# Kernel optimization log

Measured on AMD Instinct MI355X. Metric: run time of the kernel, lower is better.

## Reference

```python
import jax, jax.numpy as jnp
import numpy as np

NUM_LEVELS = 4
RADIUS = 4


def _bilinear_zeros(img, x, y):
    """Bilinear sample img (N,H,W) at absolute pixel coords x,y (N,S,S),
    zeros padding outside, matching torch grid_sample(align_corners=True,
    padding_mode='zeros') with absolute->normalized->absolute roundtrip."""
    N, H, W = img.shape
    x0 = jnp.floor(x); y0 = jnp.floor(y)
    x1 = x0 + 1.0;     y1 = y0 + 1.0
    wx1 = x - x0; wx0 = 1.0 - wx1
    wy1 = y - y0; wy0 = 1.0 - wy1
    flat = img.reshape(N, H * W)

    def gather(xi, yi):
        valid = (xi >= 0) & (xi <= W - 1) & (yi >= 0) & (yi <= H - 1)
        xc = jnp.clip(xi, 0, W - 1).astype(jnp.int32)
        yc = jnp.clip(yi, 0, H - 1).astype(jnp.int32)
        idx = (yc * W + xc).reshape(N, -1)
        v = jnp.take_along_axis(flat, idx, axis=1).reshape(xi.shape)
        return jnp.where(valid, v, jnp.zeros((), img.dtype))

    return (wy0 * wx0 * gather(x0, y0) + wy0 * wx1 * gather(x1, y0)
            + wy1 * wx0 * gather(x0, y1) + wy1 * wx1 * gather(x1, y1))


def _avg_pool2(v):
    N, H, W = v.shape
    return v.reshape(N, H // 2, 2, W // 2, 2).mean(axis=(2, 4))


def setup_inputs() -> dict:
    key = jax.random.key(0)
    k1, k2, k3 = jax.random.split(key, 3)
    B, M, C, H, W = 2, 4096, 256, 64, 64
    fmap1 = jax.random.normal(k1, (B, M, C), dtype=jnp.float32)
    fmap2 = jax.random.normal(k2, (B, C, H, W), dtype=jnp.float32)
    u = jax.random.uniform(k3, (B, M, 2), dtype=jnp.float32)
    centroids_coords = u * jnp.array([W - 1, H - 1], dtype=jnp.float32)
    return {"fmap1": fmap1, "fmap2": fmap2, "centroids_coords": centroids_coords}


def reference(fmap1, fmap2, centroids_coords):
    B, M, C = fmap1.shape
    _, _, H, W = fmap2.shape
    side = 2 * RADIUS + 1

    # correlation volume: (B, M, H, W) -> (B*M, H, W)
    corr = jnp.einsum('bmc,bchw->bmhw', fmap1, fmap2).reshape(B * M, H, W)

    d = jnp.arange(-RADIUS, RADIUS + 1, dtype=centroids_coords.dtype)
    di, dj = jnp.meshgrid(d, d, indexing='ij')
    delta = jnp.stack([di, dj], axis=-1)  # (S, S, 2): ch0 = x-offset, ch1 = y-offset

    c = centroids_coords.reshape(B * M, 1, 1, 2)
    vol = corr
    feats = []
    for lvl in range(NUM_LEVELS):
        sc = c + delta                        # (B*M, S, S, 2)
        sampled = _bilinear_zeros(vol, sc[..., 0], sc[..., 1])
        feats.append(sampled.reshape(B, M, side * side))
        c = c / 2.0
        if lvl < NUM_LEVELS - 1:
            vol = _avg_pool2(vol)
    # (B, M, num_levels*S*S) -> (B, out_channels, M)
    return jnp.concatenate(feats, axis=-1).transpose(0, 2, 1)
```

## Files before the change

kernel.cpp:

```cpp
#include <hip/hip_runtime.h>
#include <stdint.h>
#include <stddef.h>

static constexpr int Bb = 2;
static constexpr int Mq = 4096;
static constexpr int Cc = 256;
static constexpr int Hh = 64, Ww = 64;
static constexpr int Np = Hh * Ww;
static constexpr int NL1 = 1024;
static constexpr int RAD = 4;
static constexpr int SIDE = 2 * RAD + 1;
static constexpr int KPL = SIDE * SIDE;
static constexpr int NLVL = 4;
static constexpr int KTOT = NLVL * KPL;

static constexpr size_t WINBUF_B = 0;
static constexpr size_t ABF_B    = WINBUF_B + (size_t)Bb * Mq * 400 * 4;
static constexpr size_t BT_B     = ABF_B + (size_t)Bb * Mq * Cc * 2;
static constexpr size_t B1T_B    = BT_B + (size_t)Bb * Np * Cc * 2;
static constexpr size_t B2T_B    = B1T_B + (size_t)Bb * NL1 * Cc * 2;
static constexpr size_t B3T_B    = B2T_B + (size_t)Bb * 256 * Cc * 2;

typedef float floatx4 __attribute__((ext_vector_type(4)));
typedef short shortx8 __attribute__((ext_vector_type(8)));

union BfPack {
    shortx8 v;
    unsigned short u[8];
};

__device__ __forceinline__ unsigned short f2bf(float f) {
    unsigned int x = __float_as_uint(f);
    x += 0x7fffu + ((x >> 16) & 1u);
    return (unsigned short)(x >> 16);
}

__device__ __forceinline__ float bf2f(unsigned short u) {
    return __uint_as_float((unsigned int)u << 16);
}

__global__ __launch_bounds__(256)
void cvt_kernel(const float* __restrict__ f1, const float* __restrict__ f2,
                unsigned short* __restrict__ Abf, unsigned short* __restrict__ Bt,
                unsigned short* __restrict__ B1t)
{
    __shared__ float tile[64 * 132];
    const int tid = threadIdx.x;
    if (blockIdx.x < 1024) {
        const int t = blockIdx.x * 256 + tid;
        const float4 v0 = *(const float4*)(f1 + (size_t)t * 8);
        const float4 v1 = *(const float4*)(f1 + (size_t)t * 8 + 4);
        BfPack p;
        p.u[0] = f2bf(v0.x); p.u[1] = f2bf(v0.y);
        p.u[2] = f2bf(v0.z); p.u[3] = f2bf(v0.w);
        p.u[4] = f2bf(v1.x); p.u[5] = f2bf(v1.y);
        p.u[6] = f2bf(v1.z); p.u[7] = f2bf(v1.w);
        *(shortx8*)(Abf + (size_t)t * 8) = p.v;
        return;
    }
    const int bid  = blockIdx.x - 1024;
    const int b    = bid >> 7;
    const int cblk = (bid >> 5) & 3;
    const int y1   = bid & 31;

#pragma unroll
    for (int i = 0; i < 8; ++i) {
        const int v  = i * 256 + tid;
        const int c  = v >> 5;
        const int f4 = v & 31;
        *(float4*)&tile[c * 132 + f4 * 4] =
            *(const float4*)&f2[((size_t)(b * Cc + cblk * 64 + c)) * Np + y1 * 128 + f4 * 4];
    }
    __syncthreads();

#pragma unroll
    for (int i = 0; i < 4; ++i) {
        const int w  = i * 256 + tid;
        const int rp = w >> 3;
        const int cg = w & 7;
        BfPack p;
#pragma unroll
        for (int u = 0; u < 8; ++u)
            p.u[u] = f2bf(tile[(cg * 8 + u) * 132 + rp]);
        *(shortx8*)&Bt[((size_t)(b * Np + y1 * 128 + rp)) * Cc + cblk * 64 + cg * 8] = p.v;
    }

    {
        const int x1 = tid >> 3;
        const int cg = tid & 7;
        BfPack p;
#pragma unroll
        for (int u = 0; u < 8; ++u) {
            const int c = cg * 8 + u;
            const float v = 0.25f * (tile[c * 132 + 2 * x1]      + tile[c * 132 + 2 * x1 + 1]
                                   + tile[c * 132 + 64 + 2 * x1] + tile[c * 132 + 64 + 2 * x1 + 1]);
            p.u[u] = f2bf(v);
        }
        *(shortx8*)&B1t[((size_t)(b * NL1 + y1 * 32 + x1)) * Cc + cblk * 64 + cg * 8] = p.v;
    }
}

__global__ __launch_bounds__(256)
void pool23_kernel(const unsigned short* __restrict__ B1t,
                   unsigned short* __restrict__ B2t,
                   unsigned short* __restrict__ B3t)
{
    const int idx = blockIdx.x * 256 + threadIdx.x;
    if (idx < Bb * 256 * 32) {
        const int cg = idx & 31;
        const int p2 = (idx >> 5) & 255;
        const int b  = idx >> 13;
        const int y2 = p2 >> 4, x2 = p2 & 15;
        float s[8] = {0,0,0,0,0,0,0,0};
#pragma unroll
        for (int dy = 0; dy < 2; ++dy)
#pragma unroll
            for (int dx = 0; dx < 2; ++dx) {
                const int p1 = (2 * y2 + dy) * 32 + 2 * x2 + dx;
                BfPack v;
                v.v = *(const shortx8*)&B1t[((size_t)b * NL1 + p1) * Cc + cg * 8];
#pragma unroll
                for (int u = 0; u < 8; ++u) s[u] += bf2f(v.u[u]);
            }
        BfPack o;
#pragma unroll
        for (int u = 0; u < 8; ++u) o.u[u] = f2bf(0.25f * s[u]);
        *(shortx8*)&B2t[((size_t)b * 256 + p2) * Cc + cg * 8] = o.v;
    } else if (idx < Bb * 256 * 32 + Bb * 64 * 32) {
        const int i = idx - Bb * 256 * 32;
        const int cg = i & 31;
        const int p3 = (i >> 5) & 63;
        const int b  = i >> 11;
        const int y3 = p3 >> 3, x3 = p3 & 7;
        float s[8] = {0,0,0,0,0,0,0,0};
#pragma unroll
        for (int dy = 0; dy < 4; ++dy)
#pragma unroll
            for (int dx = 0; dx < 4; ++dx) {
                const int p1 = (4 * y3 + dy) * 32 + 4 * x3 + dx;
                BfPack v;
                v.v = *(const shortx8*)&B1t[((size_t)b * NL1 + p1) * Cc + cg * 8];
#pragma unroll
                for (int u = 0; u < 8; ++u) s[u] += bf2f(v.u[u]);
            }
        BfPack o;
#pragma unroll
        for (int u = 0; u < 8; ++u) o.u[u] = f2bf(0.0625f * s[u]);
        *(shortx8*)&B3t[((size_t)b * 64 + p3) * Cc + cg * 8] = o.v;
    }
}

__global__ __launch_bounds__(512)
void win4_kernel(const unsigned short* __restrict__ Abf,
                 const unsigned short* __restrict__ B0t,
                 const unsigned short* __restrict__ B1t,
                 const unsigned short* __restrict__ B2t,
                 const unsigned short* __restrict__ B3t,
                 const float* __restrict__ cent,
                 float* __restrict__ winbuf)
{
    __shared__ int qlist[128];
    __shared__ int qx0s[128], qy0s[128];
    __shared__ int qcnt;

    const int tid  = threadIdx.x;
    const int wave = tid >> 6;
    const int lane = tid & 63;
    const int lane15 = lane & 15;
    const int quad   = lane >> 4;
    const int bidx = blockIdx.x;

    int lvl, b, cell = 0, q0 = 0;
    bool binned;
    if (bidx < 512)      { lvl = 0; binned = true;  b = bidx >> 8;          cell = bidx & 255; }
    else if (bidx < 640) { lvl = 1; binned = true;  b = (bidx - 512) >> 6;  cell = (bidx - 512) & 63; }
    else if (bidx < 768) { lvl = 2; binned = false; b = (bidx - 640) >> 6;  q0 = ((bidx - 640) & 63) * 64; }
    else                 { lvl = 3; binned = false; b = (bidx - 768) >> 6;  q0 = ((bidx - 768) & 63) * 64; }

    const int w   = Ww >> lvl;
    const int npx = w * w;
    const float scale = 1.0f / (float)(1 << lvl);
    const unsigned short* Bl = (lvl == 0) ? B0t : (lvl == 1) ? B1t : (lvl == 2) ? B2t : B3t;

    int xmin = 0, ymin = 0, rh = w, rw = w, rstride = w, ntile = npx >> 4;
    int cnt;

    if (binned) {
        const int ncx  = w >> 2;
        const int binx = cell & (ncx - 1);
        const int biny = cell >> (4 - lvl);
        xmin = 4 * binx - 4; if (xmin < 0) xmin = 0;
        ymin = 4 * biny - 4; if (ymin < 0) ymin = 0;
        int xmax = 4 * binx + 8; if (xmax > w - 1) xmax = w - 1;
        int ymax = 4 * biny + 8; if (ymax > w - 1) ymax = w - 1;
        rh = ymax - ymin + 1; rw = xmax - xmin + 1;
        rstride = 13;
        ntile = (rh * 13 + 15) >> 4;

        if (tid == 0) qcnt = 0;
        __syncthreads();
#pragma unroll
        for (int i = 0; i < 8; ++i) {
            const int m = i * 512 + tid;
            const float2 cc = *(const float2*)&cent[((size_t)b * Mq + m) * 2];
            const int fx = (int)floorf(cc.x * scale);
            const int fy = (int)floorf(cc.y * scale);
            if ((fx >> 2) == binx && (fy >> 2) == biny) {
                const int idx = atomicAdd(&qcnt, 1);
                if (idx < 128) {
                    qlist[idx] = m;
                    qx0s[idx] = fx - RAD;
                    qy0s[idx] = fy - RAD;
                }
            }
        }
        __syncthreads();
        cnt = qcnt < 128 ? qcnt : 128;
    } else {
        if (tid < 64) {
            const int m = q0 + tid;
            const float2 cc = *(const float2*)&cent[((size_t)b * Mq + m) * 2];
            qlist[tid] = m;
            qx0s[tid] = (int)floorf(cc.x * scale) - RAD;
            qy0s[tid] = (int)floorf(cc.y * scale) - RAD;
        }
        __syncthreads();
        cnt = 64;
    }

    const int jt0 = wave, jt1 = wave + 8;
    const bool t0ok = jt0 < ntile;
    const bool t1ok = jt1 < ntile;
    int y0 = ymin, x0 = xmin, y1 = ymin, x1 = xmin;
    bool v0 = false, v1 = false;
    {
        const int px = jt0 * 16 + lane15;
        int py = (rstride == 13) ? ((px * 5043) >> 16) : (px >> (6 - lvl));
        const int pxx = px - py * rstride;
        v0 = t0ok && (py < rh) && (pxx < rw);
        if (py > rh - 1) py = rh - 1;
        const int pxc = pxx < rw ? pxx : rw - 1;
        y0 = ymin + py; x0 = xmin + pxc;
    }
    {
        const int px = jt1 * 16 + lane15;
        int py = (rstride == 13) ? ((px * 5043) >> 16) : (px >> (6 - lvl));
        const int pxx = px - py * rstride;
        v1 = t1ok && (py < rh) && (pxx < rw);
        if (py > rh - 1) py = rh - 1;
        const int pxc = pxx < rw ? pxx : rw - 1;
        y1 = ymin + py; x1 = xmin + pxc;
    }
    const size_t bB = (size_t)b * npx * Cc;
    const unsigned short* bp0 = Bl + bB + (size_t)(y0 * w + x0) * Cc + quad * 8;
    const unsigned short* bp1 = Bl + bB + (size_t)(y1 * w + x1) * Cc + quad * 8;

    shortx8 bfr0[8], bfr1[8];
#pragma unroll
    for (int k0 = 0; k0 < 8; ++k0)
        bfr0[k0] = *(const shortx8*)&bp0[k0 * 32];
#pragma unroll
    for (int k0 = 0; k0 < 8; ++k0)
        bfr1[k0] = *(const shortx8*)&bp1[k0 * 32];

    for (int m0 = 0; m0 < cnt; m0 += 16) {
        const int qidx = (m0 + lane15) < cnt ? (m0 + lane15) : (cnt - 1);
        const unsigned short* arow = Abf + (size_t)(b * Mq + qlist[qidx]) * Cc + quad * 8;
        shortx8 afr[8];
#pragma unroll
        for (int k0 = 0; k0 < 8; ++k0)
            afr[k0] = *(const shortx8*)&arow[k0 * 32];

        floatx4 acc0 = {0.f, 0.f, 0.f, 0.f};
        floatx4 acc1 = {0.f, 0.f, 0.f, 0.f};
        if (t0ok) {
#pragma unroll
            for (int k0 = 0; k0 < 8; ++k0)
                acc0 = __builtin_amdgcn_mfma_f32_16x16x32_bf16(afr[k0], bfr0[k0], acc0, 0, 0, 0);
        }
        if (t1ok) {
#pragma unroll
            for (int k0 = 0; k0 < 8; ++k0)
                acc1 = __builtin_amdgcn_mfma_f32_16x16x32_bf16(afr[k0], bfr1[k0], acc1, 0, 0, 0);
        }

#pragma unroll
        for (int t = 0; t < 2; ++t) {
            const bool vv = (t == 0) ? v0 : v1;
            if (!vv) continue;
            const floatx4 a = (t == 0) ? acc0 : acc1;
            const int yy = (t == 0) ? y0 : y1;
            const int xx = (t == 0) ? x0 : x1;
#pragma unroll
            for (int r = 0; r < 4; ++r) {
                const int qi = m0 + quad * 4 + r;
                if (qi < cnt) {
                    const int wy = yy - qy0s[qi];
                    const int wx = xx - qx0s[qi];
                    if ((unsigned)wy < 10u && (unsigned)wx < 10u)
                        winbuf[((size_t)b * Mq + qlist[qi]) * 400 + lvl * 100 + wy * 10 + wx] = a[r];
                }
            }
        }
    }
}

__global__ __launch_bounds__(256)
void pyr_sample_kernel(const float* __restrict__ cent,
                       const float* __restrict__ winbuf,
                       float* __restrict__ out)
{
    __shared__ float win[8][400];
    __shared__ float qcx[8], qcy[8];
    __shared__ int qx0l[8][4], qy0l[8][4];

    const int tid = threadIdx.x;
    const int b   = blockIdx.x >> 9;
    const int m0  = (blockIdx.x & 511) * 8;
    const size_t gq0 = (size_t)(b * Mq + m0);

    if (tid < 32) {
        const int q = tid >> 2, l = tid & 3;
        const float cx = cent[(gq0 + q) * 2 + 0];
        const float cy = cent[(gq0 + q) * 2 + 1];
        if (l == 0) { qcx[q] = cx; qcy[q] = cy; }
        const float scl = 1.0f / (float)(1 << l);
        qx0l[q][l] = (int)floorf(cx * scl) - RAD;
        qy0l[q][l] = (int)floorf(cy * scl) - RAD;
    }
    for (int v = tid; v < 800; v += 256) {
        const int q = (v * 41) >> 12;
        const int o = v - q * 100;
        *(float4*)&win[q][o * 4] = *(const float4*)&winbuf[(gq0 + q) * 400 + o * 4];
    }
    __syncthreads();

    for (int i = 0; i < 11; ++i) {
        const int idx = i * 256 + tid;
        if (idx >= KTOT * 8) break;
        const int q  = idx & 7;
        const int kk = idx >> 3;
        const int lvl = kk / KPL;
        const int r   = kk - lvl * KPL;
        const int di  = r / SIDE;
        const int dj  = r - di * SIDE;

        const int w = Ww >> lvl;
        const float scale = 1.0f / (float)(1 << lvl);
        const float x = qcx[q] * scale + (float)(di - RAD);
        const float y = qcy[q] * scale + (float)(dj - RAD);

        const float x0f = floorf(x), y0f = floorf(y);
        const float wx1 = x - x0f, wx0 = 1.0f - wx1;
        const float wy1 = y - y0f, wy0 = 1.0f - wy1;
        const float fmx = (float)(w - 1);
        const bool vx0 = (x0f >= 0.0f) && (x0f <= fmx);
        const bool vx1 = (x0f + 1.0f >= 0.0f) && (x0f + 1.0f <= fmx);
        const bool vy0 = (y0f >= 0.0f) && (y0f <= fmx);
        const bool vy1 = (y0f + 1.0f >= 0.0f) && (y0f + 1.0f <= fmx);

        const int ix0 = (int)x0f, iy0 = (int)y0f;

        const float* buf = &win[q][lvl * 100];
        const int ox = qx0l[q][lvl], oy = qy0l[q][lvl];
        const int cx0 = ix0 - ox, cx1 = cx0 + 1;
        const int cy0r = iy0 - oy, cy1r = cy0r + 1;
        const float g00 = (vx0 && vy0) ? buf[cy0r * 10 + cx0] : 0.0f;
        const float g10 = (vx1 && vy0) ? buf[cy0r * 10 + cx1] : 0.0f;
        const float g01 = (vx0 && vy1) ? buf[cy1r * 10 + cx0] : 0.0f;
        const float g11 = (vx1 && vy1) ? buf[cy1r * 10 + cx1] : 0.0f;

        out[((size_t)b * KTOT + kk) * Mq + m0 + q] =
            wy0 * (wx0 * g00 + wx1 * g10) + wy1 * (wx0 * g01 + wx1 * g11);
    }
}

extern "C" void kernel_launch(void* const* d_in, const int* in_sizes, int n_in,
                              void* d_out, int out_size, void* d_ws, size_t ws_size,
                              hipStream_t stream)
{
    const float* fmap1 = (const float*)d_in[0];
    const float* fmap2 = (const float*)d_in[1];
    const float* cent  = (const float*)d_in[2];
    char* ws = (char*)d_ws;
    float* winbuf = (float*)(ws + WINBUF_B);
    unsigned short* Abf = (unsigned short*)(ws + ABF_B);
    unsigned short* Bt  = (unsigned short*)(ws + BT_B);
    unsigned short* B1t = (unsigned short*)(ws + B1T_B);
    unsigned short* B2t = (unsigned short*)(ws + B2T_B);
    unsigned short* B3t = (unsigned short*)(ws + B3T_B);
    float* out = (float*)d_out;

    cvt_kernel<<<1280, 256, 0, stream>>>(fmap1, fmap2, Abf, Bt, B1t);

    pool23_kernel<<<80, 256, 0, stream>>>(B1t, B2t, B3t);

    win4_kernel<<<896, 512, 0, stream>>>(Abf, Bt, B1t, B2t, B3t, cent, winbuf);

    pyr_sample_kernel<<<Bb * Mq / 8, 256, 0, stream>>>(cent, winbuf, out);
}
```

Before: 132.0 us.

## Stage pyramid region tiles in LDS and bin level-2 queries spatially

The window-correlation kernel now loads each block's 13x13 feature-map region cooperatively into shared memory. MFMA B-fragments are read from LDS instead of being held as per-lane global loads in registers. Level 2 moves from dense full-map blocks to spatially binned blocks, split into two halves of the query set, and the query-list capacity grows to 384. This cuts redundant global traffic and register pressure and shrinks the grid. The cost is a large LDS footprint per block, which limits blocks per CU, plus an extra staging phase.

Result: no change. 133.3 us (+1.0%).

```diff
diff --git a/kernel.cpp b/kernel.cpp
--- a/kernel.cpp
+++ b/kernel.cpp
@@ -159,8 +159,8 @@
                  const float* __restrict__ cent,
                  float* __restrict__ winbuf)
 {
-    __shared__ int qlist[128];
-    __shared__ int qx0s[128], qy0s[128];
+    __shared__ unsigned short reg[169 * 264];
+    __shared__ int qlist[384], qx0s[384], qy0s[384];
     __shared__ int qcnt;
 
     const int tid  = threadIdx.x;
@@ -170,20 +170,20 @@
     const int quad   = lane >> 4;
     const int bidx = blockIdx.x;
 
-    int lvl, b, cell = 0, q0 = 0;
+    int lvl, b, cell = 0, q0 = 0, half = -1;
     bool binned;
-    if (bidx < 512)      { lvl = 0; binned = true;  b = bidx >> 8;          cell = bidx & 255; }
-    else if (bidx < 640) { lvl = 1; binned = true;  b = (bidx - 512) >> 6;  cell = (bidx - 512) & 63; }
-    else if (bidx < 768) { lvl = 2; binned = false; b = (bidx - 640) >> 6;  q0 = ((bidx - 640) & 63) * 64; }
-    else                 { lvl = 3; binned = false; b = (bidx - 768) >> 6;  q0 = ((bidx - 768) & 63) * 64; }
+    if (bidx < 512)      { lvl = 0; binned = true;  b = bidx >> 8;  cell = bidx & 255; }
+    else if (bidx < 640) { lvl = 1; binned = true;  b = (bidx - 512) >> 6; cell = (bidx - 512) & 63; }
+    else if (bidx < 704) { lvl = 2; binned = true;  const int t = bidx - 640; b = t >> 5; cell = (t & 31) >> 1; half = t & 1; }
+    else                 { lvl = 3; binned = false; const int t = bidx - 704; b = t >> 6; q0 = (t & 63) * 64; }
 
     const int w   = Ww >> lvl;
     const int npx = w * w;
     const float scale = 1.0f / (float)(1 << lvl);
     const unsigned short* Bl = (lvl == 0) ? B0t : (lvl == 1) ? B1t : (lvl == 2) ? B2t : B3t;
-
-    int xmin = 0, ymin = 0, rh = w, rw = w, rstride = w, ntile = npx >> 4;
-    int cnt;
+    const unsigned short* bsrc = Bl + (size_t)b * npx * Cc;
+
+    int xmin = 0, ymin = 0, rh = w, rw = w;
 
     if (binned) {
         const int ncx  = w >> 2;
@@ -194,28 +194,28 @@
         int xmax = 4 * binx + 8; if (xmax > w - 1) xmax = w - 1;
         int ymax = 4 * biny + 8; if (ymax > w - 1) ymax = w - 1;
         rh = ymax - ymin + 1; rw = xmax - xmin + 1;
-        rstride = 13;
-        ntile = (rh * 13 + 15) >> 4;
 
         if (tid == 0) qcnt = 0;
         __syncthreads();
+        float2 cbuf[8];
+#pragma unroll
+        for (int i = 0; i < 8; ++i)
+            cbuf[i] = *(const float2*)&cent[((size_t)b * Mq + i * 512 + tid) * 2];
 #pragma unroll
         for (int i = 0; i < 8; ++i) {
             const int m = i * 512 + tid;
-            const float2 cc = *(const float2*)&cent[((size_t)b * Mq + m) * 2];
-            const int fx = (int)floorf(cc.x * scale);
-            const int fy = (int)floorf(cc.y * scale);
-            if ((fx >> 2) == binx && (fy >> 2) == biny) {
+            const int fx = (int)floorf(cbuf[i].x * scale);
+            const int fy = (int)floorf(cbuf[i].y * scale);
+            if ((fx >> 2) == binx && (fy >> 2) == biny &&
+                (half < 0 || (m >> 11) == half)) {
                 const int idx = atomicAdd(&qcnt, 1);
-                if (idx < 128) {
+                if (idx < 384) {
                     qlist[idx] = m;
                     qx0s[idx] = fx - RAD;
                     qy0s[idx] = fy - RAD;
                 }
             }
         }
-        __syncthreads();
-        cnt = qcnt < 128 ? qcnt : 128;
     } else {
         if (tid < 64) {
             const int m = q0 + tid;
@@ -224,47 +224,64 @@
             qx0s[tid] = (int)floorf(cc.x * scale) - RAD;
             qy0s[tid] = (int)floorf(cc.y * scale) - RAD;
         }
-        __syncthreads();
-        cnt = 64;
-    }
-
+    }
+
+    {
+        const int total = rh * 13 * 32;
+        shortx8 sbuf[11];
+        int saddr[11];
+        bool sok[11];
+#pragma unroll
+        for (int it = 0; it < 11; ++it) {
+            const int v   = it * 512 + tid;
+            const int pix = v >> 5;
+            const int g   = v & 31;
+            const int ry  = (pix * 5043) >> 16;
+            const int rx  = pix - ry * 13;
+            const bool ok = (v < total) && (ry < rh) && (rx < rw);
+            sok[it] = ok;
+            saddr[it] = pix * 264 + g * 8;
+            const int gy = ymin + (ry < rh ? ry : rh - 1);
+            const int gx = xmin + (rx < rw ? rx : rw - 1);
+            sbuf[it] = ok ? *(const shortx8*)&bsrc[((size_t)(gy * w + gx)) * Cc + g * 8]
+                          : shortx8{0, 0, 0, 0, 0, 0, 0, 0};
+        }
+#pragma unroll
+        for (int it = 0; it < 11; ++it)
+            if (sok[it]) *(shortx8*)&reg[saddr[it]] = sbuf[it];
+    }
+    __syncthreads();
+    const int cnt = binned ? (qcnt < 384 ? qcnt : 384) : 64;
+
+    const int ntile = ((rh - 1) * 13 + rw + 15) >> 4;
     const int jt0 = wave, jt1 = wave + 8;
     const bool t0ok = jt0 < ntile;
     const bool t1ok = jt1 < ntile;
     int y0 = ymin, x0 = xmin, y1 = ymin, x1 = xmin;
     bool v0 = false, v1 = false;
+    int lb0, lb1;
     {
-        const int px = jt0 * 16 + lane15;
-        int py = (rstride == 13) ? ((px * 5043) >> 16) : (px >> (6 - lvl));
-        const int pxx = px - py * rstride;
+        const int px  = jt0 * 16 + lane15;
+        const int py  = (px * 5043) >> 16;
+        const int pxx = px - py * 13;
         v0 = t0ok && (py < rh) && (pxx < rw);
-        if (py > rh - 1) py = rh - 1;
-        const int pxc = pxx < rw ? pxx : rw - 1;
-        y0 = ymin + py; x0 = xmin + pxc;
+        y0 = ymin + (py < rh ? py : rh - 1);
+        x0 = xmin + (pxx < rw ? pxx : rw - 1);
+        lb0 = (px <= 168 ? px : 168) * 264 + quad * 8;
     }
     {
-        const int px = jt1 * 16 + lane15;
-        int py = (rstride == 13) ? ((px * 5043) >> 16) : (px >> (6 - lvl));
-        const int pxx = px - py * rstride;
+        const int px  = jt1 * 16 + lane15;
+        const int py  = (px * 5043) >> 16;
+        const int pxx = px - py * 13;
         v1 = t1ok && (py < rh) && (pxx < rw);
-        if (py > rh - 1) py = rh - 1;
-        const int pxc = pxx < rw ? pxx : rw - 1;
-        y1 = ymin + py; x1 = xmin + pxc;
-    }
-    const size_t bB = (size_t)b * npx * Cc;
-    const unsigned short* bp0 = Bl + bB + (size_t)(y0 * w + x0) * Cc + quad * 8;
-    const unsigned short* bp1 = Bl + bB + (size_t)(y1 * w + x1) * Cc + quad * 8;
-
-    shortx8 bfr0[8], bfr1[8];
-#pragma unroll
-    for (int k0 = 0; k0 < 8; ++k0)
-        bfr0[k0] = *(const shortx8*)&bp0[k0 * 32];
-#pragma unroll
-    for (int k0 = 0; k0 < 8; ++k0)
-        bfr1[k0] = *(const shortx8*)&bp1[k0 * 32];
+        y1 = ymin + (py < rh ? py : rh - 1);
+        x1 = xmin + (pxx < rw ? pxx : rw - 1);
+        lb1 = (px <= 168 ? px : 168) * 264 + quad * 8;
+    }
 
     for (int m0 = 0; m0 < cnt; m0 += 16) {
-        const int qidx = (m0 + lane15) < cnt ? (m0 + lane15) : (cnt - 1);
+        const int qi16 = m0 + lane15;
+        const int qidx = qi16 < cnt ? qi16 : cnt - 1;
         const unsigned short* arow = Abf + (size_t)(b * Mq + qlist[qidx]) * Cc + quad * 8;
         shortx8 afr[8];
 #pragma unroll
@@ -276,12 +293,14 @@
         if (t0ok) {
 #pragma unroll
             for (int k0 = 0; k0 < 8; ++k0)
-                acc0 = __builtin_amdgcn_mfma_f32_16x16x32_bf16(afr[k0], bfr0[k0], acc0, 0, 0, 0);
+                acc0 = __builtin_amdgcn_mfma_f32_16x16x32_bf16(
+                    afr[k0], *(const shortx8*)&reg[lb0 + k0 * 32], acc0, 0, 0, 0);
         }
         if (t1ok) {
 #pragma unroll
             for (int k0 = 0; k0 < 8; ++k0)
-                acc1 = __builtin_amdgcn_mfma_f32_16x16x32_bf16(afr[k0], bfr1[k0], acc1, 0, 0, 0);
+                acc1 = __builtin_amdgcn_mfma_f32_16x16x32_bf16(
+                    afr[k0], *(const shortx8*)&reg[lb1 + k0 * 32], acc1, 0, 0, 0);
         }
 
 #pragma unroll
@@ -395,7 +414,7 @@
 
     pool23_kernel<<<80, 256, 0, stream>>>(B1t, B2t, B3t);
 
-    win4_kernel<<<896, 512, 0, stream>>>(Abf, Bt, B1t, B2t, B3t, cent, winbuf);
+    win4_kernel<<<832, 512, 0, stream>>>(Abf, Bt, B1t, B2t, B3t, cent, winbuf);
 
     pyr_sample_kernel<<<Bb * Mq / 8, 256, 0, stream>>>(cent, winbuf, out);
 }
```
